# Kernel tuning notes

Measured on AMD Instinct MI355X. Metric: run time of the kernel, lower is better.

The kernel has to match this reference:

```python
import jax, jax.numpy as jnp
import numpy as np

N = 25000        # nodes
E = 400000       # edges (avg 16 neighbors)
C1 = 8           # output_size (scalar channels into TP)
COUT = 16        # channels_out
LMAX = 2
NB = 8           # number_of_basis
RMAX = 5.0       # max_radius
EMB = 16         # atom embedding dim
NATOM = 10
WNUM = (LMAX + 1) * C1 * COUT                 # per-edge TP weights (parity-shared, k0 paths)
TOTAL_DIM = 2 * COUT * (1 + 3 + 9)            # both parities x ranks 0..2 -> 416


def setup_inputs() -> dict:
    key = jax.random.key(0)
    ks = jax.random.split(key, 12)
    rn = lambda i, shape, s=1.0: jax.random.normal(ks[i], shape, jnp.float32) * s
    pos = rn(0, (N, 3)) * 3.0
    A = jax.random.randint(ks[1], (N,), 0, NATOM)
    batch = jnp.zeros((N,), jnp.int32)                       # single graph
    edge_src = jax.random.randint(ks[2], (E,), 0, N)
    # avoid self-edges (zero-length vectors)
    edge_dst = (edge_src + jax.random.randint(ks[3], (E,), 1, N)) % N
    edge_shifts = jnp.zeros((E, 3), jnp.float32)
    cell = jnp.eye(3, dtype=jnp.float32)[None] * 10.0        # [1,3,3]
    emb_table = rn(4, (NATOM, EMB))
    atom_w1 = rn(5, (EMB, 64), EMB ** -0.5)
    atom_b1 = jnp.zeros((64,), jnp.float32)
    atom_w2 = rn(6, (64, C1), 64 ** -0.5)
    atom_b2 = jnp.zeros((C1,), jnp.float32)
    fc_w1 = rn(7, (NB, 64), NB ** -0.5)
    fc_b1 = jnp.zeros((64,), jnp.float32)
    fc_w2 = rn(8, (64, 64), 64 ** -0.5)
    fc_b2 = jnp.zeros((64,), jnp.float32)
    fc_w3 = rn(9, (64, WNUM), 64 ** -0.5)
    fc_b3 = jnp.zeros((WNUM,), jnp.float32)
    return dict(pos=pos, A=A, batch=batch, edge_src=edge_src, edge_dst=edge_dst,
                edge_shifts=edge_shifts, cell=cell, emb_table=emb_table,
                atom_w1=atom_w1, atom_b1=atom_b1, atom_w2=atom_w2, atom_b2=atom_b2,
                fc_w1=fc_w1, fc_b1=fc_b1, fc_w2=fc_w2, fc_b2=fc_b2, fc_w3=fc_w3, fc_b3=fc_b3)


def reference(pos, A, batch, edge_src, edge_dst, edge_shifts, cell, emb_table,
              atom_w1, atom_b1, atom_w2, atom_b2,
              fc_w1, fc_b1, fc_w2, fc_b2, fc_w3, fc_b3):
    num_edges = edge_src.shape[0]
    num_nodes = pos.shape[0]
    # edge geometry (PBC shift)
    edge_cells = cell[batch[edge_src]]                                   # [E,3,3]
    shift_vecs = jnp.einsum('ni,nij->nj', edge_shifts, edge_cells)
    edge_vec = pos[edge_dst] - pos[edge_src] + shift_vecs                # [E,3]
    edge_length = jnp.sqrt(jnp.sum(edge_vec * edge_vec, axis=1) + 1e-12)
    # per-node scalar features -> gathered to edges
    Ai = jax.nn.silu(emb_table[A] @ atom_w1 + atom_b1) @ atom_w2 + atom_b2  # [N,C1]
    Ai_e = Ai[edge_src]                                                    # [E,C1]
    # edge_rank_powers (normalized): rank-0 scalar 1, rank-1 u, rank-2 u\otimes u
    u = edge_vec / edge_length[:, None]
    # radial basis: e3nn soft_one_hot_linspace (gaussian, cutoff) * sqrt(NB)
    values = jnp.linspace(0.0, RMAX, NB + 2)[1:-1]
    step = RMAX / (NB + 1)
    diff = (edge_length[:, None] - values) / step
    emb = (jnp.exp(-diff * diff) / 1.12) * (NB ** 0.5)                     # [E,NB]
    # radial MLP -> per-edge TP weights
    h = jax.nn.silu(emb @ fc_w1 + fc_b1)
    h = jax.nn.silu(h @ fc_w2 + fc_b2)
    w = (h @ fc_w3 + fc_b3).reshape(num_edges, LMAX + 1, C1, COUT)
    # sparse cartesian O(3) tensor product (k0 paths; only (0,0)x(0,L)->(0,L) nonzero
    # since all x1 L>=1 and parity-1 blocks are zero by construction)
    b0 = jnp.einsum('eco,ec->eo', w[:, 0], Ai_e)                           # [E,COUT]
    b1 = jnp.einsum('eco,ec,ei->eoi', w[:, 1], Ai_e, u)                    # [E,COUT,3]
    b2 = jnp.einsum('eco,ec,ei,ej->eoij', w[:, 2], Ai_e, u, u)             # [E,COUT,3,3]
    feats = jnp.concatenate([b0, b1.reshape(num_edges, -1), b2.reshape(num_edges, -1)], axis=1)
    edge_features = jnp.concatenate([feats, jnp.zeros_like(feats)], axis=1)  # pseudo blocks = 0
    # scatter-sum to destination nodes, normalize by global avg num neighbors
    out = jax.ops.segment_sum(edge_features, edge_dst, num_segments=num_nodes)
    avg_num_neighbors = jnp.maximum(jnp.float32(num_edges) / jnp.float32(num_nodes), 1e-8)
    return out / avg_num_neighbors
```

## Files before the change

### kernel.cpp

```cpp
#include <hip/hip_runtime.h>
#include <math.h>

#define NN 25000
#define NE 400000
#define TD 416
#define TCAP 46080
#define NROWS (TCAP * 10)
#define PLH 64
#define NCAP 64
#define GROWS 32

typedef __attribute__((ext_vector_type(8))) __bf16 bf16x8;
typedef __attribute__((ext_vector_type(4))) _Float16 f16x4;
typedef __attribute__((ext_vector_type(4))) float f32x4;

__device__ __forceinline__ float silu_f(float x) {
    return x * __builtin_amdgcn_rcpf(1.0f + __expf(-x));
}

__global__ __launch_bounds__(256) void prep_count_k(
    const float* __restrict__ emb_table,
    const float* __restrict__ aw1, const float* __restrict__ ab1,
    const float* __restrict__ aw2, const float* __restrict__ ab2,
    const float* __restrict__ fw1, const float* __restrict__ fb1,
    const float* __restrict__ fw2,
    const float* __restrict__ fw3, const float* __restrict__ fb3,
    __bf16* __restrict__ w1a, __bf16* __restrict__ w2a,
    __bf16* __restrict__ w3ta, float* __restrict__ b3t,
    const int* __restrict__ esrc, const int* __restrict__ edst,
    const int* __restrict__ A,
    int* __restrict__ cnt_dst, int* __restrict__ cnt_t,
    int* __restrict__ tlist) {
    const int tid = threadIdx.x;
    if (blockIdx.x < 64) {
        __shared__ float s_ai[80];
        if (tid < 10) {
            float acc[8];
#pragma unroll
            for (int o = 0; o < 8; ++o) acc[o] = ab2[o];
            for (int j = 0; j < 64; ++j) {
                float h = ab1[j];
#pragma unroll
                for (int i = 0; i < 16; ++i) h += emb_table[tid * 16 + i] * aw1[i * 64 + j];
                h = silu_f(h);
#pragma unroll
                for (int o = 0; o < 8; ++o) acc[o] += h * aw2[j * 8 + o];
            }
#pragma unroll
            for (int o = 0; o < 8; ++o) s_ai[tid * 8 + o] = acc[o];
        }
        __syncthreads();
        for (int i = blockIdx.x * 256 + tid; i < 37344; i += 64 * 256) {
            if (i < 2048) {
                int m = i >> 9, r = i & 511, lane = r >> 3, j = r & 7;
                int k = (lane >> 4) * 8 + j, ch = m * 16 + (lane & 15);
                float v = (k < 8) ? fw1[k * 64 + ch] : ((k == 8) ? fb1[ch] : 0.0f);
                w1a[i] = (__bf16)v;
            } else if (i < 6144) {
                int q = i - 2048;
                int mk = q >> 9, lane = (q >> 3) & 63, j = q & 7;
                int m = mk >> 1, kt = mk & 1;
                int k = kt * 32 + (lane >> 4) * 8 + j, ch = m * 16 + (lane & 15);
                w2a[q] = (__bf16)fw2[k * 64 + ch];
            } else if (i < 36864) {
                int q = i - 6144;
                int tmk = q >> 9, lane = (q >> 3) & 63, j = q & 7;
                int kt = tmk & 1, tm = tmk >> 1;
                int t = tm / 3, m = tm - t * 3;
                int k = kt * 32 + (lane >> 4) * 8 + j, ch = m * 16 + (lane & 15);
                int l = ch >> 4, o = ch & 15;
                float s = 0.f;
#pragma unroll
                for (int c = 0; c < 8; ++c)
                    s += s_ai[t * 8 + c] * fw3[k * 384 + l * 128 + c * 16 + o];
                w3ta[q] = (__bf16)s;
            } else {
                int q2 = i - 36864;
                int t = q2 / 48, ch = q2 - t * 48;
                int l = ch >> 4, o = ch & 15;
                float s = 0.f;
#pragma unroll
                for (int c = 0; c < 8; ++c)
                    s += s_ai[t * 8 + c] * fb3[l * 128 + c * 16 + o];
                b3t[q2] = s;
            }
        }
    } else {
        __shared__ int lcnt[10];
        __shared__ int gbase[10];
        if (tid < 10) lcnt[tid] = 0;
        __syncthreads();
        int e = (blockIdx.x - 64) * 256 + tid;
        int t = 0, lr = 0, rank = 0;
        bool valid = e < NE;
        if (valid) {
            rank = atomicAdd(&cnt_dst[edst[e]], 1);
            t = A[esrc[e]];
            lr = atomicAdd(&lcnt[t], 1);
        }
        __syncthreads();
        if (tid < 10) gbase[tid] = atomicAdd(&cnt_t[tid], lcnt[tid]);
        __syncthreads();
        if (valid) tlist[t * TCAP + gbase[t] + lr] = e | (rank << 19);
    }
}

__global__ __launch_bounds__(64, 4) void edge_k(
    const int* __restrict__ tlist, const int* __restrict__ cnt_t,
    const int* __restrict__ esrc, const int* __restrict__ edst,
    const float* __restrict__ pos, const float* __restrict__ shifts,
    const float* __restrict__ cell, const int* __restrict__ batch,
    const __bf16* __restrict__ w1a, const __bf16* __restrict__ w2a,
    const __bf16* __restrict__ w3ta,
    const float* __restrict__ fb2, const float* __restrict__ b3t,
    _Float16* __restrict__ payload) {
    __shared__ __bf16 embuf[64 * 36];
    __shared__ __bf16 h1buf[16 * 72];
    __shared__ __bf16 h2buf[16 * 72];
    __shared__ int pbuf[64];
    const int lane = threadIdx.x;
    const int base = blockIdx.x * 64;
    const int t_blk = base / TCAP;
    const int nval = cnt_t[t_blk];
    const int local = base - t_blk * TCAP;
    if (local >= nval) return;

    int idx = min(local + lane, nval - 1);
    const int pk = tlist[t_blk * TCAP + idx];
    const int eid = pk & 0x7FFFF;
    const int rank = pk >> 19;

    const int src = esrc[eid], dstn = edst[eid];
    const int pd = dstn * NCAP + rank;
    pbuf[lane] = pd;
    const int b = batch[src];
    const float* cb = cell + b * 9;
    const float sh0 = shifts[eid * 3 + 0], sh1 = shifts[eid * 3 + 1], sh2 = shifts[eid * 3 + 2];
    float vx = pos[dstn * 3 + 0] - pos[src * 3 + 0] + sh0 * cb[0] + sh1 * cb[3] + sh2 * cb[6];
    float vy = pos[dstn * 3 + 1] - pos[src * 3 + 1] + sh0 * cb[1] + sh1 * cb[4] + sh2 * cb[7];
    float vz = pos[dstn * 3 + 2] - pos[src * 3 + 2] + sh0 * cb[2] + sh1 * cb[5] + sh2 * cb[8];
    const float l2 = vx * vx + vy * vy + vz * vz + 1e-12f;
    const float il = __builtin_amdgcn_rsqf(l2);
    const float len = l2 * il;
    {
        union { float f[4]; uint4 u; } uu;
        uu.f[0] = vx * il; uu.f[1] = vy * il; uu.f[2] = vz * il; uu.f[3] = 0.f;
        *(uint4*)(payload + (size_t)pd * PLH + 48) = uu.u;
    }

    bf16x8 er0;
#pragma unroll
    for (int k = 0; k < 8; ++k) {
        float d = (len - (5.0f * (float)(k + 1) / 9.0f)) * 1.8f;
        er0[k] = (__bf16)(__expf(-d * d) * 2.525381361380528f);
    }
    bf16x8 er1 = {};
    er1[0] = (__bf16)1.0f;
    bf16x8 zz = {};
    *(bf16x8*)&embuf[lane * 36 + 0]  = er0;
    *(bf16x8*)&embuf[lane * 36 + 8]  = er1;
    *(bf16x8*)&embuf[lane * 36 + 16] = zz;
    *(bf16x8*)&embuf[lane * 36 + 24] = zz;

    bf16x8 a1[4], a2[8], a3[6];
#pragma unroll
    for (int m = 0; m < 4; ++m) a1[m] = *(const bf16x8*)(w1a + (m * 64 + lane) * 8);
#pragma unroll
    for (int i = 0; i < 8; ++i) a2[i] = *(const bf16x8*)(w2a + (i * 64 + lane) * 8);
#pragma unroll
    for (int i = 0; i < 6; ++i)
        a3[i] = *(const bf16x8*)(w3ta + ((size_t)(t_blk * 6 + i) * 64 + lane) * 8);
    const int qr = (lane >> 4) * 4;
    const int q8 = (lane >> 4) * 8;
    f32x4 bias2[4], bias3[3];
#pragma unroll
    for (int m = 0; m < 4; ++m) bias2[m] = *(const f32x4*)(fb2 + m * 16 + qr);
#pragma unroll
    for (int m = 0; m < 3; ++m) bias3[m] = *(const f32x4*)(b3t + t_blk * 48 + m * 16 + qr);
    __syncthreads();

    const float SC = (float)NN / (float)NE;
    const int colrow = lane & 15;
#pragma unroll 1
    for (int n = 0; n < 4; ++n) {
        const int erow = n * 16 + colrow;
        bf16x8 b1 = *(bf16x8*)&embuf[erow * 36 + q8];
#pragma unroll
        for (int m = 0; m < 4; ++m) {
            f32x4 c = {0.f, 0.f, 0.f, 0.f};
            c = __builtin_amdgcn_mfma_f32_16x16x32_bf16(a1[m], b1, c, 0, 0, 0);
            __bf16 hp[4];
#pragma unroll
            for (int r = 0; r < 4; ++r) hp[r] = (__bf16)silu_f(c[r]);
            *(uint2*)&h1buf[colrow * 72 + m * 16 + qr] = *(uint2*)hp;
        }
        __syncthreads();
        bf16x8 b20 = *(bf16x8*)&h1buf[colrow * 72 + q8];
        bf16x8 b21 = *(bf16x8*)&h1buf[colrow * 72 + 32 + q8];
#pragma unroll
        for (int m = 0; m < 4; ++m) {
            f32x4 c = bias2[m];
            c = __builtin_amdgcn_mfma_f32_16x16x32_bf16(a2[m * 2 + 0], b20, c, 0, 0, 0);
            c = __builtin_amdgcn_mfma_f32_16x16x32_bf16(a2[m * 2 + 1], b21, c, 0, 0, 0);
            __bf16 hp[4];
#pragma unroll
            for (int r = 0; r < 4; ++r) hp[r] = (__bf16)silu_f(c[r]);
            *(uint2*)&h2buf[colrow * 72 + m * 16 + qr] = *(uint2*)hp;
        }
        __syncthreads();
        const int prow = pbuf[erow];
        bf16x8 b30 = *(bf16x8*)&h2buf[colrow * 72 + q8];
        bf16x8 b31 = *(bf16x8*)&h2buf[colrow * 72 + 32 + q8];
#pragma unroll
        for (int m = 0; m < 3; ++m) {
            f32x4 c = bias3[m];
            c = __builtin_amdgcn_mfma_f32_16x16x32_bf16(a3[m * 2 + 0], b30, c, 0, 0, 0);
            c = __builtin_amdgcn_mfma_f32_16x16x32_bf16(a3[m * 2 + 1], b31, c, 0, 0, 0);
            f16x4 hp;
#pragma unroll
            for (int r = 0; r < 4; ++r) hp[r] = (_Float16)(c[r] * SC);
            *(f16x4*)(payload + (size_t)prow * PLH + m * 16 + qr) = hp;
        }
    }
}

__global__ __launch_bounds__(256) void gather_k(const int* __restrict__ cnt_dst,
                                                const _Float16* __restrict__ payload,
                                                float* __restrict__ out) {
    __shared__ __align__(16) _Float16 sp_s[GROWS][72];
    __shared__ float sfac[GROWS][16];
    const int n = blockIdx.x;
    const int tid = threadIdx.x;
    const int lo = n * NCAP;
    const int cnt = cnt_dst[n];
    int voff = 0, foff = 0;
    if (tid < 16) { voff = tid; foff = 0; }
    else if (tid < 64) { int q = tid - 16; voff = 16 + q / 3; foff = 1 + q % 3; }
    else if (tid < 208) { int q = tid - 64; voff = 32 + q / 9; foff = 4 + q % 9; }
    float acc = 0.f;
    for (int p0 = 0; p0 < cnt; p0 += GROWS) {
        const int m = min(GROWS, cnt - p0);
        if (tid < m * 8) {
            int r = tid >> 3, q = tid & 7;
            ((uint4*)&sp_s[r][0])[q] = ((const uint4*)(payload + (size_t)(lo + p0 + r) * PLH))[q];
        }
        __syncthreads();
        for (int idx = tid; idx < m * 16; idx += 256) {
            int r = idx >> 4, f = idx & 15;
            if (f < 13) {
                const float* uf = (const float*)&sp_s[r][48];
                float v;
                if (f == 0) v = 1.0f;
                else if (f < 4) v = uf[f - 1];
                else { int g = f - 4; v = uf[g / 3] * uf[g % 3]; }
                sfac[r][f] = v;
            }
        }
        __syncthreads();
        if (tid < 208)
            for (int r = 0; r < m; ++r)
                acc += (float)sp_s[r][voff] * sfac[r][foff];
        __syncthreads();
    }
    if (tid < 208) {
        out[(size_t)n * TD + tid] = acc;
        out[(size_t)n * TD + 208 + tid] = 0.f;
    }
}

extern "C" void kernel_launch(void* const* d_in, const int* in_sizes, int n_in,
                              void* d_out, int out_size, void* d_ws, size_t ws_size,
                              hipStream_t stream) {
    const float* pos       = (const float*)d_in[0];
    const int*   A         = (const int*)d_in[1];
    const int*   batch     = (const int*)d_in[2];
    const int*   esrc      = (const int*)d_in[3];
    const int*   edst      = (const int*)d_in[4];
    const float* shifts    = (const float*)d_in[5];
    const float* cell      = (const float*)d_in[6];
    const float* emb_table = (const float*)d_in[7];
    const float* aw1       = (const float*)d_in[8];
    const float* ab1       = (const float*)d_in[9];
    const float* aw2       = (const float*)d_in[10];
    const float* ab2       = (const float*)d_in[11];
    const float* fw1       = (const float*)d_in[12];
    const float* fb1       = (const float*)d_in[13];
    const float* fw2       = (const float*)d_in[14];
    const float* fb2       = (const float*)d_in[15];
    const float* fw3       = (const float*)d_in[16];
    const float* fb3       = (const float*)d_in[17];
    float* out = (float*)d_out;

    char* base = (char*)d_ws;
    __bf16* w1a    = (__bf16*)(base + 0);
    __bf16* w2a    = (__bf16*)(base + 4096);
    __bf16* w3ta   = (__bf16*)(base + 12288);
    float*  b3t    = (float*)(base + 73728);
    int* cnt_dst   = (int*)(base + 75648);
    int* cnt_t     = (int*)(base + 175680);
    int* tlist     = (int*)(base + 175808);
    _Float16* payload = (_Float16*)(base + 2019072);

    hipMemsetAsync(cnt_dst, 0, 100160, stream);
    prep_count_k<<<64 + (NE + 255) / 256, 256, 0, stream>>>(
        emb_table, aw1, ab1, aw2, ab2, fw1, fb1, fw2, fw3, fb3,
        w1a, w2a, w3ta, b3t, esrc, edst, A, cnt_dst, cnt_t, tlist);
    edge_k<<<NROWS / 64, 64, 0, stream>>>(tlist, cnt_t, esrc, edst, pos, shifts, cell, batch,
                                          w1a, w2a, w3ta, fb2, b3t, payload);
    gather_k<<<NN, 256, 0, stream>>>(cnt_dst, payload, out);
}
```

Baseline: 187.8 us.

## Process four edge groups per block to amortize weight loads and prefetch geometry

Each edge_k block now handles four 64-edge groups rather than one. This amortizes the per-block loading of MLP weight fragments and biases across more edges, and it software-pipelines the gather of the next group's positions and shifts. The embedding buffer shrinks to 8 bf16 per edge, with the constant bias row supplied from registers. An extra zero store pads payload columns 56-63. The grid is four times smaller and occupancy hints are removed, so latency hiding depends more on ILP and less on the number of waves, and an extra barrier per inner iteration is added.

```diff
diff --git a/kernel.cpp b/kernel.cpp
--- a/kernel.cpp
+++ b/kernel.cpp
@@ -9,6 +9,8 @@
 #define PLH 64
 #define NCAP 64
 #define GROWS 32
+#define NGRP 4
+#define BPT (TCAP / (NGRP * 64))
 
 typedef __attribute__((ext_vector_type(8))) __bf16 bf16x8;
 typedef __attribute__((ext_vector_type(4))) _Float16 f16x4;
@@ -105,7 +107,7 @@
     }
 }
 
-__global__ __launch_bounds__(64, 4) void edge_k(
+__global__ __launch_bounds__(64) void edge_k(
     const int* __restrict__ tlist, const int* __restrict__ cnt_t,
     const int* __restrict__ esrc, const int* __restrict__ edst,
     const float* __restrict__ pos, const float* __restrict__ shifts,
@@ -114,53 +116,28 @@
     const __bf16* __restrict__ w3ta,
     const float* __restrict__ fb2, const float* __restrict__ b3t,
     _Float16* __restrict__ payload) {
-    __shared__ __bf16 embuf[64 * 36];
+    __shared__ __bf16 embuf[2][64 * 8];
     __shared__ __bf16 h1buf[16 * 72];
     __shared__ __bf16 h2buf[16 * 72];
-    __shared__ int pbuf[64];
+    __shared__ int pbuf[2][64];
     const int lane = threadIdx.x;
-    const int base = blockIdx.x * 64;
-    const int t_blk = base / TCAP;
+    const int t_blk = blockIdx.x / BPT;
+    const int local0 = (blockIdx.x - t_blk * BPT) * (NGRP * 64);
     const int nval = cnt_t[t_blk];
-    const int local = base - t_blk * TCAP;
-    if (local >= nval) return;
-
-    int idx = min(local + lane, nval - 1);
-    const int pk = tlist[t_blk * TCAP + idx];
-    const int eid = pk & 0x7FFFF;
-    const int rank = pk >> 19;
-
-    const int src = esrc[eid], dstn = edst[eid];
-    const int pd = dstn * NCAP + rank;
-    pbuf[lane] = pd;
-    const int b = batch[src];
-    const float* cb = cell + b * 9;
-    const float sh0 = shifts[eid * 3 + 0], sh1 = shifts[eid * 3 + 1], sh2 = shifts[eid * 3 + 2];
-    float vx = pos[dstn * 3 + 0] - pos[src * 3 + 0] + sh0 * cb[0] + sh1 * cb[3] + sh2 * cb[6];
-    float vy = pos[dstn * 3 + 1] - pos[src * 3 + 1] + sh0 * cb[1] + sh1 * cb[4] + sh2 * cb[7];
-    float vz = pos[dstn * 3 + 2] - pos[src * 3 + 2] + sh0 * cb[2] + sh1 * cb[5] + sh2 * cb[8];
-    const float l2 = vx * vx + vy * vy + vz * vz + 1e-12f;
-    const float il = __builtin_amdgcn_rsqf(l2);
-    const float len = l2 * il;
-    {
-        union { float f[4]; uint4 u; } uu;
-        uu.f[0] = vx * il; uu.f[1] = vy * il; uu.f[2] = vz * il; uu.f[3] = 0.f;
-        *(uint4*)(payload + (size_t)pd * PLH + 48) = uu.u;
-    }
-
-    bf16x8 er0;
-#pragma unroll
-    for (int k = 0; k < 8; ++k) {
-        float d = (len - (5.0f * (float)(k + 1) / 9.0f)) * 1.8f;
-        er0[k] = (__bf16)(__expf(-d * d) * 2.525381361380528f);
-    }
-    bf16x8 er1 = {};
-    er1[0] = (__bf16)1.0f;
-    bf16x8 zz = {};
-    *(bf16x8*)&embuf[lane * 36 + 0]  = er0;
-    *(bf16x8*)&embuf[lane * 36 + 8]  = er1;
-    *(bf16x8*)&embuf[lane * 36 + 16] = zz;
-    *(bf16x8*)&embuf[lane * 36 + 24] = zz;
+    if (local0 >= nval) return;
+
+    int pk[NGRP], srcv[NGRP], dstv[NGRP];
+#pragma unroll
+    for (int g = 0; g < NGRP; ++g) {
+        int idx = min(local0 + g * 64 + lane, nval - 1);
+        pk[g] = tlist[t_blk * TCAP + idx];
+    }
+#pragma unroll
+    for (int g = 0; g < NGRP; ++g) {
+        int eid = pk[g] & 0x7FFFF;
+        srcv[g] = esrc[eid];
+        dstv[g] = edst[eid];
+    }
 
     bf16x8 a1[4], a2[8], a3[6];
 #pragma unroll
@@ -170,58 +147,115 @@
 #pragma unroll
     for (int i = 0; i < 6; ++i)
         a3[i] = *(const bf16x8*)(w3ta + ((size_t)(t_blk * 6 + i) * 64 + lane) * 8);
-    const int qr = (lane >> 4) * 4;
-    const int q8 = (lane >> 4) * 8;
+    const int q = lane >> 4;
+    const int qr = q * 4;
+    const int q8 = q * 8;
+    const int colrow = lane & 15;
     f32x4 bias2[4], bias3[3];
 #pragma unroll
     for (int m = 0; m < 4; ++m) bias2[m] = *(const f32x4*)(fb2 + m * 16 + qr);
 #pragma unroll
     for (int m = 0; m < 3; ++m) bias3[m] = *(const f32x4*)(b3t + t_blk * 48 + m * 16 + qr);
-    __syncthreads();
+
+    bf16x8 bone = {};
+    bone[0] = (__bf16)1.0f;
+
+    float psh[2][3], pps[2][3], ppd[2][3];
+    int bb[2];
+#define GEOLOAD(buf, g)                                                        \
+    {                                                                          \
+        int eid_ = pk[g] & 0x7FFFF;                                            \
+        psh[buf][0] = shifts[eid_ * 3 + 0];                                    \
+        psh[buf][1] = shifts[eid_ * 3 + 1];                                    \
+        psh[buf][2] = shifts[eid_ * 3 + 2];                                    \
+        pps[buf][0] = pos[srcv[g] * 3 + 0];                                    \
+        pps[buf][1] = pos[srcv[g] * 3 + 1];                                    \
+        pps[buf][2] = pos[srcv[g] * 3 + 2];                                    \
+        ppd[buf][0] = pos[dstv[g] * 3 + 0];                                    \
+        ppd[buf][1] = pos[dstv[g] * 3 + 1];                                    \
+        ppd[buf][2] = pos[dstv[g] * 3 + 2];                                    \
+        bb[buf] = batch[srcv[g]];                                              \
+    }
+    GEOLOAD(0, 0);
 
     const float SC = (float)NN / (float)NE;
-    const int colrow = lane & 15;
+    const uint4 z4 = {0u, 0u, 0u, 0u};
+
+#pragma unroll
+    for (int g = 0; g < NGRP; ++g) {
+        if (g + 1 < NGRP) GEOLOAD((g + 1) & 1, g + 1);
+        const int gb = g & 1;
+        const int rank = pk[g] >> 19;
+        const int pd = dstv[g] * NCAP + rank;
+        pbuf[gb][lane] = pd;
+        const float* cb = cell + bb[gb] * 9;
+        const float sh0 = psh[gb][0], sh1 = psh[gb][1], sh2 = psh[gb][2];
+        float vx = ppd[gb][0] - pps[gb][0] + sh0 * cb[0] + sh1 * cb[3] + sh2 * cb[6];
+        float vy = ppd[gb][1] - pps[gb][1] + sh0 * cb[1] + sh1 * cb[4] + sh2 * cb[7];
+        float vz = ppd[gb][2] - pps[gb][2] + sh0 * cb[2] + sh1 * cb[5] + sh2 * cb[8];
+        const float l2 = vx * vx + vy * vy + vz * vz + 1e-12f;
+        const float il = __builtin_amdgcn_rsqf(l2);
+        const float len = l2 * il;
+        {
+            union { float f[4]; uint4 u; } uu;
+            uu.f[0] = vx * il; uu.f[1] = vy * il; uu.f[2] = vz * il; uu.f[3] = 0.f;
+            *(uint4*)(payload + (size_t)pd * PLH + 48) = uu.u;
+            *(uint4*)(payload + (size_t)pd * PLH + 56) = z4;
+        }
+        bf16x8 er0;
+#pragma unroll
+        for (int k = 0; k < 8; ++k) {
+            float d = (len - (5.0f * (float)(k + 1) / 9.0f)) * 1.8f;
+            er0[k] = (__bf16)(__expf(-d * d) * 2.525381361380528f);
+        }
+        *(bf16x8*)&embuf[gb][lane * 8] = er0;
+        __syncthreads();
+
 #pragma unroll 1
-    for (int n = 0; n < 4; ++n) {
-        const int erow = n * 16 + colrow;
-        bf16x8 b1 = *(bf16x8*)&embuf[erow * 36 + q8];
-#pragma unroll
-        for (int m = 0; m < 4; ++m) {
-            f32x4 c = {0.f, 0.f, 0.f, 0.f};
-            c = __builtin_amdgcn_mfma_f32_16x16x32_bf16(a1[m], b1, c, 0, 0, 0);
-            __bf16 hp[4];
-#pragma unroll
-            for (int r = 0; r < 4; ++r) hp[r] = (__bf16)silu_f(c[r]);
-            *(uint2*)&h1buf[colrow * 72 + m * 16 + qr] = *(uint2*)hp;
-        }
-        __syncthreads();
-        bf16x8 b20 = *(bf16x8*)&h1buf[colrow * 72 + q8];
-        bf16x8 b21 = *(bf16x8*)&h1buf[colrow * 72 + 32 + q8];
-#pragma unroll
-        for (int m = 0; m < 4; ++m) {
-            f32x4 c = bias2[m];
-            c = __builtin_amdgcn_mfma_f32_16x16x32_bf16(a2[m * 2 + 0], b20, c, 0, 0, 0);
-            c = __builtin_amdgcn_mfma_f32_16x16x32_bf16(a2[m * 2 + 1], b21, c, 0, 0, 0);
-            __bf16 hp[4];
-#pragma unroll
-            for (int r = 0; r < 4; ++r) hp[r] = (__bf16)silu_f(c[r]);
-            *(uint2*)&h2buf[colrow * 72 + m * 16 + qr] = *(uint2*)hp;
-        }
-        __syncthreads();
-        const int prow = pbuf[erow];
-        bf16x8 b30 = *(bf16x8*)&h2buf[colrow * 72 + q8];
-        bf16x8 b31 = *(bf16x8*)&h2buf[colrow * 72 + 32 + q8];
-#pragma unroll
-        for (int m = 0; m < 3; ++m) {
-            f32x4 c = bias3[m];
-            c = __builtin_amdgcn_mfma_f32_16x16x32_bf16(a3[m * 2 + 0], b30, c, 0, 0, 0);
-            c = __builtin_amdgcn_mfma_f32_16x16x32_bf16(a3[m * 2 + 1], b31, c, 0, 0, 0);
-            f16x4 hp;
-#pragma unroll
-            for (int r = 0; r < 4; ++r) hp[r] = (_Float16)(c[r] * SC);
-            *(f16x4*)(payload + (size_t)prow * PLH + m * 16 + qr) = hp;
-        }
-    }
+        for (int n = 0; n < 4; ++n) {
+            const int erow = n * 16 + colrow;
+            bf16x8 bd = *(bf16x8*)&embuf[gb][erow * 8];
+            bf16x8 b1 = (q == 0) ? bd : bone;
+#pragma unroll
+            for (int m = 0; m < 4; ++m) {
+                f32x4 c = {0.f, 0.f, 0.f, 0.f};
+                c = __builtin_amdgcn_mfma_f32_16x16x32_bf16(a1[m], b1, c, 0, 0, 0);
+                __bf16 hp[4];
+#pragma unroll
+                for (int r = 0; r < 4; ++r) hp[r] = (__bf16)silu_f(c[r]);
+                *(uint2*)&h1buf[colrow * 72 + m * 16 + qr] = *(uint2*)hp;
+            }
+            __syncthreads();
+            bf16x8 b20 = *(bf16x8*)&h1buf[colrow * 72 + q8];
+            bf16x8 b21 = *(bf16x8*)&h1buf[colrow * 72 + 32 + q8];
+#pragma unroll
+            for (int m = 0; m < 4; ++m) {
+                f32x4 c = bias2[m];
+                c = __builtin_amdgcn_mfma_f32_16x16x32_bf16(a2[m * 2 + 0], b20, c, 0, 0, 0);
+                c = __builtin_amdgcn_mfma_f32_16x16x32_bf16(a2[m * 2 + 1], b21, c, 0, 0, 0);
+                __bf16 hp[4];
+#pragma unroll
+                for (int r = 0; r < 4; ++r) hp[r] = (__bf16)silu_f(c[r]);
+                *(uint2*)&h2buf[colrow * 72 + m * 16 + qr] = *(uint2*)hp;
+            }
+            __syncthreads();
+            const int prow = pbuf[gb][erow];
+            bf16x8 b30 = *(bf16x8*)&h2buf[colrow * 72 + q8];
+            bf16x8 b31 = *(bf16x8*)&h2buf[colrow * 72 + 32 + q8];
+#pragma unroll
+            for (int m = 0; m < 3; ++m) {
+                f32x4 c = bias3[m];
+                c = __builtin_amdgcn_mfma_f32_16x16x32_bf16(a3[m * 2 + 0], b30, c, 0, 0, 0);
+                c = __builtin_amdgcn_mfma_f32_16x16x32_bf16(a3[m * 2 + 1], b31, c, 0, 0, 0);
+                f16x4 hp;
+#pragma unroll
+                for (int r = 0; r < 4; ++r) hp[r] = (_Float16)(c[r] * SC);
+                *(f16x4*)(payload + (size_t)prow * PLH + m * 16 + qr) = hp;
+            }
+            __syncthreads();
+        }
+    }
+#undef GEOLOAD
 }
 
 __global__ __launch_bounds__(256) void gather_k(const int* __restrict__ cnt_dst,
@@ -305,7 +339,7 @@
     prep_count_k<<<64 + (NE + 255) / 256, 256, 0, stream>>>(
         emb_table, aw1, ab1, aw2, ab2, fw1, fb1, fw2, fw3, fb3,
         w1a, w2a, w3ta, b3t, esrc, edst, A, cnt_dst, cnt_t, tlist);
-    edge_k<<<NROWS / 64, 64, 0, stream>>>(tlist, cnt_t, esrc, edst, pos, shifts, cell, batch,
-                                          w1a, w2a, w3ta, fb2, b3t, payload);
+    edge_k<<<10 * BPT, 64, 0, stream>>>(tlist, cnt_t, esrc, edst, pos, shifts, cell, batch,
+                                        w1a, w2a, w3ta, fb2, b3t, payload);
     gather_k<<<NN, 256, 0, stream>>>(cnt_dst, payload, out);
 }
```

Result: slower. 195.7 us (+4.2%).

## Compute edge vectors during bucketing and pass packed records to edge kernel

Applied to the files above, without the earlier changes.

The counting/bucketing pass now computes the edge displacement vector and stores it together with the packed destination slot as an int4 record. The edge kernel then reads that one coalesced record instead of doing random gathers of esrc, edst, pos, shifts, cell and batch. The embedding LDS buffer shrinks to 8 values per edge, and the constant bias-one operand is built in registers rather than stored to LDS. In exchange the list buffer grows fourfold, and the edge kernel now also zeros the padding half of the payload slot and drops its occupancy hint.

```diff
diff --git a/kernel.cpp b/kernel.cpp
--- a/kernel.cpp
+++ b/kernel.cpp
@@ -9,6 +9,7 @@
 #define PLH 64
 #define NCAP 64
 #define GROWS 32
+#define BPT (TCAP / 64)
 
 typedef __attribute__((ext_vector_type(8))) __bf16 bf16x8;
 typedef __attribute__((ext_vector_type(4))) _Float16 f16x4;
@@ -29,8 +30,10 @@
     __bf16* __restrict__ w3ta, float* __restrict__ b3t,
     const int* __restrict__ esrc, const int* __restrict__ edst,
     const int* __restrict__ A,
+    const float* __restrict__ pos, const float* __restrict__ shifts,
+    const float* __restrict__ cell, const int* __restrict__ batch,
     int* __restrict__ cnt_dst, int* __restrict__ cnt_t,
-    int* __restrict__ tlist) {
+    int4* __restrict__ tlist4) {
     const int tid = threadIdx.x;
     if (blockIdx.x < 64) {
         __shared__ float s_ai[80];
@@ -91,61 +94,66 @@
         if (tid < 10) lcnt[tid] = 0;
         __syncthreads();
         int e = (blockIdx.x - 64) * 256 + tid;
-        int t = 0, lr = 0, rank = 0;
+        int t = 0, lr = 0;
+        int4 rec;
         bool valid = e < NE;
         if (valid) {
-            rank = atomicAdd(&cnt_dst[edst[e]], 1);
-            t = A[esrc[e]];
+            const int dst = edst[e];
+            const int src = esrc[e];
+            int rank = atomicAdd(&cnt_dst[dst], 1);
+            t = A[src];
             lr = atomicAdd(&lcnt[t], 1);
+            const int b = batch[src];
+            const float* cb = cell + b * 9;
+            const float sh0 = shifts[e * 3 + 0], sh1 = shifts[e * 3 + 1], sh2 = shifts[e * 3 + 2];
+            float vx = pos[dst * 3 + 0] - pos[src * 3 + 0] + sh0 * cb[0] + sh1 * cb[3] + sh2 * cb[6];
+            float vy = pos[dst * 3 + 1] - pos[src * 3 + 1] + sh0 * cb[1] + sh1 * cb[4] + sh2 * cb[7];
+            float vz = pos[dst * 3 + 2] - pos[src * 3 + 2] + sh0 * cb[2] + sh1 * cb[5] + sh2 * cb[8];
+            rec.x = __float_as_int(vx);
+            rec.y = __float_as_int(vy);
+            rec.z = __float_as_int(vz);
+            rec.w = (dst << 6) | rank;
         }
         __syncthreads();
         if (tid < 10) gbase[tid] = atomicAdd(&cnt_t[tid], lcnt[tid]);
         __syncthreads();
-        if (valid) tlist[t * TCAP + gbase[t] + lr] = e | (rank << 19);
-    }
-}
-
-__global__ __launch_bounds__(64, 4) void edge_k(
-    const int* __restrict__ tlist, const int* __restrict__ cnt_t,
-    const int* __restrict__ esrc, const int* __restrict__ edst,
-    const float* __restrict__ pos, const float* __restrict__ shifts,
-    const float* __restrict__ cell, const int* __restrict__ batch,
+        if (valid) tlist4[t * TCAP + gbase[t] + lr] = rec;
+    }
+}
+
+__global__ __launch_bounds__(64) void edge_k(
+    const int4* __restrict__ tlist4, const int* __restrict__ cnt_t,
     const __bf16* __restrict__ w1a, const __bf16* __restrict__ w2a,
     const __bf16* __restrict__ w3ta,
     const float* __restrict__ fb2, const float* __restrict__ b3t,
     _Float16* __restrict__ payload) {
-    __shared__ __bf16 embuf[64 * 36];
+    __shared__ __bf16 embuf[64 * 8];
     __shared__ __bf16 h1buf[16 * 72];
     __shared__ __bf16 h2buf[16 * 72];
     __shared__ int pbuf[64];
     const int lane = threadIdx.x;
-    const int base = blockIdx.x * 64;
-    const int t_blk = base / TCAP;
+    const int t_blk = blockIdx.x / BPT;
+    const int local = (blockIdx.x - t_blk * BPT) * 64;
     const int nval = cnt_t[t_blk];
-    const int local = base - t_blk * TCAP;
     if (local >= nval) return;
 
-    int idx = min(local + lane, nval - 1);
-    const int pk = tlist[t_blk * TCAP + idx];
-    const int eid = pk & 0x7FFFF;
-    const int rank = pk >> 19;
-
-    const int src = esrc[eid], dstn = edst[eid];
-    const int pd = dstn * NCAP + rank;
+    const int idx = min(local + lane, nval - 1);
+    const int4 rec = tlist4[t_blk * TCAP + idx];
+    const float vx = __int_as_float(rec.x);
+    const float vy = __int_as_float(rec.y);
+    const float vz = __int_as_float(rec.z);
+    const int pd = rec.w;
     pbuf[lane] = pd;
-    const int b = batch[src];
-    const float* cb = cell + b * 9;
-    const float sh0 = shifts[eid * 3 + 0], sh1 = shifts[eid * 3 + 1], sh2 = shifts[eid * 3 + 2];
-    float vx = pos[dstn * 3 + 0] - pos[src * 3 + 0] + sh0 * cb[0] + sh1 * cb[3] + sh2 * cb[6];
-    float vy = pos[dstn * 3 + 1] - pos[src * 3 + 1] + sh0 * cb[1] + sh1 * cb[4] + sh2 * cb[7];
-    float vz = pos[dstn * 3 + 2] - pos[src * 3 + 2] + sh0 * cb[2] + sh1 * cb[5] + sh2 * cb[8];
+
     const float l2 = vx * vx + vy * vy + vz * vz + 1e-12f;
     const float il = __builtin_amdgcn_rsqf(l2);
     const float len = l2 * il;
     {
+        const uint4 z4 = {0u, 0u, 0u, 0u};
         union { float f[4]; uint4 u; } uu;
         uu.f[0] = vx * il; uu.f[1] = vy * il; uu.f[2] = vz * il; uu.f[3] = 0.f;
         *(uint4*)(payload + (size_t)pd * PLH + 48) = uu.u;
+        *(uint4*)(payload + (size_t)pd * PLH + 56) = z4;
     }
 
     bf16x8 er0;
@@ -154,13 +162,7 @@
         float d = (len - (5.0f * (float)(k + 1) / 9.0f)) * 1.8f;
         er0[k] = (__bf16)(__expf(-d * d) * 2.525381361380528f);
     }
-    bf16x8 er1 = {};
-    er1[0] = (__bf16)1.0f;
-    bf16x8 zz = {};
-    *(bf16x8*)&embuf[lane * 36 + 0]  = er0;
-    *(bf16x8*)&embuf[lane * 36 + 8]  = er1;
-    *(bf16x8*)&embuf[lane * 36 + 16] = zz;
-    *(bf16x8*)&embuf[lane * 36 + 24] = zz;
+    *(bf16x8*)&embuf[lane * 8] = er0;
 
     bf16x8 a1[4], a2[8], a3[6];
 #pragma unroll
@@ -170,21 +172,26 @@
 #pragma unroll
     for (int i = 0; i < 6; ++i)
         a3[i] = *(const bf16x8*)(w3ta + ((size_t)(t_blk * 6 + i) * 64 + lane) * 8);
-    const int qr = (lane >> 4) * 4;
-    const int q8 = (lane >> 4) * 8;
+    const int q = lane >> 4;
+    const int qr = q * 4;
+    const int q8 = q * 8;
+    const int colrow = lane & 15;
     f32x4 bias2[4], bias3[3];
 #pragma unroll
     for (int m = 0; m < 4; ++m) bias2[m] = *(const f32x4*)(fb2 + m * 16 + qr);
 #pragma unroll
     for (int m = 0; m < 3; ++m) bias3[m] = *(const f32x4*)(b3t + t_blk * 48 + m * 16 + qr);
+
+    bf16x8 bone = {};
+    bone[0] = (__bf16)1.0f;
     __syncthreads();
 
     const float SC = (float)NN / (float)NE;
-    const int colrow = lane & 15;
 #pragma unroll 1
     for (int n = 0; n < 4; ++n) {
         const int erow = n * 16 + colrow;
-        bf16x8 b1 = *(bf16x8*)&embuf[erow * 36 + q8];
+        bf16x8 bd = *(bf16x8*)&embuf[erow * 8];
+        bf16x8 b1 = (q == 0) ? bd : bone;
 #pragma unroll
         for (int m = 0; m < 4; ++m) {
             f32x4 c = {0.f, 0.f, 0.f, 0.f};
@@ -298,14 +305,14 @@
     float*  b3t    = (float*)(base + 73728);
     int* cnt_dst   = (int*)(base + 75648);
     int* cnt_t     = (int*)(base + 175680);
-    int* tlist     = (int*)(base + 175808);
-    _Float16* payload = (_Float16*)(base + 2019072);
+    int4* tlist4   = (int4*)(base + 175808);
+    _Float16* payload = (_Float16*)(base + 7548672);
 
     hipMemsetAsync(cnt_dst, 0, 100160, stream);
     prep_count_k<<<64 + (NE + 255) / 256, 256, 0, stream>>>(
         emb_table, aw1, ab1, aw2, ab2, fw1, fb1, fw2, fw3, fb3,
-        w1a, w2a, w3ta, b3t, esrc, edst, A, cnt_dst, cnt_t, tlist);
-    edge_k<<<NROWS / 64, 64, 0, stream>>>(tlist, cnt_t, esrc, edst, pos, shifts, cell, batch,
-                                          w1a, w2a, w3ta, fb2, b3t, payload);
+        w1a, w2a, w3ta, b3t, esrc, edst, A, pos, shifts, cell, batch,
+        cnt_dst, cnt_t, tlist4);
+    edge_k<<<10 * BPT, 64, 0, stream>>>(tlist4, cnt_t, w1a, w2a, w3ta, fb2, b3t, payload);
     gather_k<<<NN, 256, 0, stream>>>(cnt_dst, payload, out);
 }
```

Result: faster. 180.5 us (-3.9%).
